# Optimization experiments

Hardware: AMD Instinct MI355X
Metric: run time of the kernel (lower is better)

Reference implementation:

```python
import jax, jax.numpy as jnp
from jax import lax
import numpy as np

B, T, ID, HD = 64, 256, 512, 1024

def setup_inputs() -> dict:
    key = jax.random.key(0)
    ks = jax.random.split(key, 5)
    s_i = 1.0 / np.sqrt(ID)
    s_h = 1.0 / np.sqrt(HD)
    return {
        'x': jax.random.normal(ks[0], (B, T, ID), jnp.float32),
        'Wi': jax.random.uniform(ks[1], (ID, 4 * HD), jnp.float32, -s_i, s_i),
        'bi': jax.random.uniform(ks[2], (4 * HD,), jnp.float32, -s_i, s_i),
        'Wh': jax.random.uniform(ks[3], (HD, 4 * HD), jnp.float32, -s_h, s_h),
        'bh': jax.random.uniform(ks[4], (4 * HD,), jnp.float32, -s_h, s_h),
    }

def reference(x, Wi, bi, Wh, bh):
    # x: [B, T, ID]; Wi: [ID, 4H]; Wh: [HD, 4H]
    b, t, _ = x.shape
    hd = Wh.shape[0]
    # Precompute input-to-hidden contribution for all timesteps: [T, B, 4H]
    gates_x = jnp.swapaxes(jnp.einsum('bti,ih->bth', x, Wi) + bi, 0, 1)

    def step(carry, gx):
        h, c = carry
        g = gx + h @ Wh + bh  # [B, 4H]
        f, i, a, o = jnp.split(g, 4, axis=-1)  # chunk order: F, I, A, O
        f = jax.nn.sigmoid(f)
        i = jax.nn.sigmoid(i)
        a = jnp.tanh(a)
        o = jax.nn.sigmoid(o)
        c = f * c + i * a
        h = o * jnp.tanh(c)
        return (h, c), h

    h0 = jnp.zeros((b, hd), x.dtype)
    c0 = jnp.zeros((b, hd), x.dtype)
    (hT, cT), hs = lax.scan(step, (h0, c0), gates_x)
    Q_all = jnp.swapaxes(hs, 0, 1)  # [B, T, HD]
    return (Q_all, hT, cT)
```

## Files before the change

### kernel.cpp

```cpp
#include <hip/hip_runtime.h>
#include <hip/hip_bf16.h>


#define B_  64
#define T_  256
#define ID_ 512
#define HD_ 1024
#define NG_ 4096
#define M1_ (B_ * T_)
#define NBLK 128
#define UPB  8

typedef __bf16 bf16x8 __attribute__((ext_vector_type(8)));
typedef float  f32x4  __attribute__((ext_vector_type(4)));
typedef int    i32x4  __attribute__((ext_vector_type(4)));
typedef int    i32x2  __attribute__((ext_vector_type(2)));
typedef short  s16x4  __attribute__((ext_vector_type(4)));

using bf16 = __hip_bfloat16;

__device__ __forceinline__ float sigmoid_fast(float x) {
    return 1.0f / (1.0f + __expf(-x));
}
__device__ __forceinline__ float tanh_fast(float x) {
    return 1.0f - 2.0f / (__expf(2.0f * x) + 1.0f);
}
__device__ __forceinline__ unsigned short bf16_bits(float x) {
    union { bf16 h; unsigned short u; } cv;
    cv.h = __float2bfloat16(x);
    return cv.u;
}
__device__ __forceinline__ bf16x8 as_bf16x8(i32x4 v) {
    union { i32x4 i; bf16x8 h; } cv;
    cv.i = v;
    return cv.h;
}

__device__ __forceinline__ void issue8(i32x4* dst, const bf16* gbase) {
    asm volatile(
        "global_load_dwordx4 %0, %8, off sc0 sc1\n\t"
        "global_load_dwordx4 %1, %8, off offset:64 sc0 sc1\n\t"
        "global_load_dwordx4 %2, %8, off offset:128 sc0 sc1\n\t"
        "global_load_dwordx4 %3, %8, off offset:192 sc0 sc1\n\t"
        "global_load_dwordx4 %4, %8, off offset:256 sc0 sc1\n\t"
        "global_load_dwordx4 %5, %8, off offset:320 sc0 sc1\n\t"
        "global_load_dwordx4 %6, %8, off offset:384 sc0 sc1\n\t"
        "global_load_dwordx4 %7, %8, off offset:448 sc0 sc1"
        : "=&v"(dst[0]), "=&v"(dst[1]), "=&v"(dst[2]), "=&v"(dst[3]),
          "=&v"(dst[4]), "=&v"(dst[5]), "=&v"(dst[6]), "=&v"(dst[7])
        : "v"(gbase));
}

__global__ __launch_bounds__(256) void prep_kernel(
    const float* __restrict__ x, const float* __restrict__ Wi,
    const float* __restrict__ Wh, bf16* __restrict__ xb,
    bf16* __restrict__ wiT, bf16* __restrict__ whT,
    bf16* __restrict__ hbuf, int* __restrict__ flags) {
    const int tid = blockIdx.x * 256 + threadIdx.x;

    if (tid < NBLK * 4 * 16) flags[tid] = 0;
    if (tid < (B_ * HD_) / 4)
        *reinterpret_cast<s16x4*>(hbuf + (size_t)tid * 4) = s16x4{0, 0, 0, 0};

    const float4 v = reinterpret_cast<const float4*>(x)[tid];
    bf16 tmp[4] = { __float2bfloat16(v.x), __float2bfloat16(v.y),
                    __float2bfloat16(v.z), __float2bfloat16(v.w) };
    *reinterpret_cast<s16x4*>(xb + 4 * (size_t)tid) =
        *reinterpret_cast<s16x4*>(tmp);

    {
        const int n = tid >> 9, k = tid & 511;
        wiT[tid] = __float2bfloat16(Wi[(size_t)k * NG_ + n]);
    }
    for (int e = 0; e < 2; ++e) {
        const int idx = 2 * tid + e;
        const int n = idx >> 10, k = idx & 1023;
        whT[idx] = __float2bfloat16(Wh[(size_t)k * NG_ + n]);
    }
}

__global__ __launch_bounds__(256) void gates_gemm_kernel(
    const bf16* __restrict__ xb, const bf16* __restrict__ wiT,
    const float* __restrict__ bi, const float* __restrict__ bh,
    bf16* __restrict__ gates3) {
    __shared__ __align__(16) bf16 As[128 * 40];
    __shared__ __align__(16) bf16 Bs[128 * 40];
    const int tid  = threadIdx.x;
    const int lane = tid & 63, wave = tid >> 6;
    const int wm = wave >> 1, wn = wave & 1;
    const int l15 = lane & 15, quad = lane >> 4;
    const int row0 = blockIdx.x * 128, col0 = blockIdx.y * 128;

    f32x4 acc[4][4];
    for (int i = 0; i < 4; ++i)
        for (int j = 0; j < 4; ++j) acc[i][j] = f32x4{0.f, 0.f, 0.f, 0.f};

    for (int kt = 0; kt < ID_ / 32; ++kt) {
        const int k0 = kt * 32;
        for (int L = tid; L < 512; L += 256) {
            const int r = L >> 2, s = L & 3;
            *reinterpret_cast<i32x4*>(&As[r * 40 + s * 8]) =
                *reinterpret_cast<const i32x4*>(xb + (size_t)(row0 + r) * ID_ + k0 + s * 8);
            *reinterpret_cast<i32x4*>(&Bs[r * 40 + s * 8]) =
                *reinterpret_cast<const i32x4*>(wiT + (size_t)(col0 + r) * ID_ + k0 + s * 8);
        }
        __syncthreads();
        bf16x8 af[4], bfv[4];
        for (int mt = 0; mt < 4; ++mt)
            af[mt] = *reinterpret_cast<const bf16x8*>(
                &As[(wm * 64 + mt * 16 + l15) * 40 + quad * 8]);
        for (int nt = 0; nt < 4; ++nt)
            bfv[nt] = *reinterpret_cast<const bf16x8*>(
                &Bs[(wn * 64 + nt * 16 + l15) * 40 + quad * 8]);
        for (int mt = 0; mt < 4; ++mt)
            for (int nt = 0; nt < 4; ++nt)
                acc[mt][nt] = __builtin_amdgcn_mfma_f32_16x16x32_bf16(
                    af[mt], bfv[nt], acc[mt][nt], 0, 0, 0);
        __syncthreads();
    }
    for (int mt = 0; mt < 4; ++mt) {
        for (int nt = 0; nt < 4; ++nt) {
            const int cg = col0 + wn * 64 + nt * 16 + l15;
            const int g = cg >> 10, u = cg & 1023;
            const int blk = u >> 3, jl = u & 7;
            const int lcol = g * 8 + jl;
            const int nt2 = lcol >> 4, q2 = (lcol >> 2) & 3, r2 = lcol & 3;
            const int e = nt2 * 4 + r2;
            const float bias = bi[cg] + bh[cg];
            for (int r = 0; r < 4; ++r) {
                const int rg = row0 + wm * 64 + mt * 16 + quad * 4 + r;
                const int b = rg >> 8, t = rg & 255;
                const int tid2 = (b >> 4) * 64 + q2 * 16 + (b & 15);
                gates3[(((size_t)t * NBLK + blk) * 256 + tid2) * 8 + e] =
                    __float2bfloat16(acc[mt][nt][r] + bias);
            }
        }
    }
}

__global__ __launch_bounds__(256, 1) void lstm_persistent_kernel(
    const bf16* __restrict__ gates3, const bf16* __restrict__ whT,
    bf16* __restrict__ hbuf, float* __restrict__ out, int* __restrict__ flags) {
    __shared__ __align__(16) bf16 whs[32 * 2 * 64 * 8];
    const int tid  = threadIdx.x;
    const int lane = tid & 63, w = tid >> 6;
    const int l15 = lane & 15, quad = lane >> 4;
    const int blk = blockIdx.x;

    for (int c = tid; c < 4096; c += 256) {
        const int kk = c >> 7, sel = (c >> 6) & 1, ln = c & 63;
        const int m = sel * 16 + (ln & 15);
        const size_t wrow = (size_t)((m >> 3) * HD_ + blk * UPB + (m & 7));
        const int col = (ln >> 4) * 8 + kk * 32;
        *reinterpret_cast<i32x4*>(whs + (size_t)c * 8) =
            *reinterpret_cast<const i32x4*>(whT + wrow * HD_ + col);
    }
    __syncthreads();

    const bf16* wb = whs + (size_t)lane * 8;

    const int jl0 = 4 * (quad & 1) + 2 * (quad >> 1);
    const int b = w * 16 + l15;
    float c0 = 0.f, c1 = 0.f;

    const int* pollp = flags + (lane << 1);

    bf16x8 gx_next = *reinterpret_cast<const bf16x8*>(
        gates3 + ((size_t)blk * 256 + tid) * 8);

    for (int t = 0; t < T_; ++t) {
        const bf16* hin  = hbuf + (size_t)(t & 1) * (B_ * HD_);
        bf16*       hout = hbuf + (size_t)((t + 1) & 1) * (B_ * HD_);
        const bf16x8 gx = gx_next;

        if (t > 0) {
            if (w == 0) {
                for (;;) {
                    i32x2 f = *reinterpret_cast<const volatile i32x2*>(pollp);
                    if (f.x >= t && f.y >= t) break;
                    __builtin_amdgcn_s_sleep(2);
                }
            }
            asm volatile("s_barrier" ::: "memory");
        }

        f32x4 a0e = f32x4{0.f, 0.f, 0.f, 0.f};
        f32x4 a0o = f32x4{0.f, 0.f, 0.f, 0.f};
        f32x4 a1e = f32x4{0.f, 0.f, 0.f, 0.f};
        f32x4 a1o = f32x4{0.f, 0.f, 0.f, 0.f};

        const bf16* hb_base = hin + (size_t)b * HD_ + quad * 8;
        i32x4 hbA[8], hbB[8];

        auto consume8 = [&](const i32x4* hbg, const int kkb) {
#pragma unroll
            for (int i = 0; i < 8; i += 2) {
                const int kk = kkb + i;
                const bf16x8 w0e = *reinterpret_cast<const bf16x8*>(wb + (size_t)kk * 1024);
                const bf16x8 w1e = *reinterpret_cast<const bf16x8*>(wb + (size_t)kk * 1024 + 512);
                const bf16x8 w0o = *reinterpret_cast<const bf16x8*>(wb + (size_t)(kk + 1) * 1024);
                const bf16x8 w1o = *reinterpret_cast<const bf16x8*>(wb + (size_t)(kk + 1) * 1024 + 512);
                a0e = __builtin_amdgcn_mfma_f32_16x16x32_bf16(w0e, as_bf16x8(hbg[i]), a0e, 0, 0, 0);
                a1e = __builtin_amdgcn_mfma_f32_16x16x32_bf16(w1e, as_bf16x8(hbg[i]), a1e, 0, 0, 0);
                a0o = __builtin_amdgcn_mfma_f32_16x16x32_bf16(w0o, as_bf16x8(hbg[i + 1]), a0o, 0, 0, 0);
                a1o = __builtin_amdgcn_mfma_f32_16x16x32_bf16(w1o, as_bf16x8(hbg[i + 1]), a1o, 0, 0, 0);
            }
        };

        issue8(hbA, hb_base);
        issue8(hbB, hb_base + 8 * 32);
        asm volatile("s_waitcnt vmcnt(8)" ::: "memory");
        __builtin_amdgcn_sched_barrier(0);
        consume8(hbA, 0);
        issue8(hbA, hb_base + 16 * 32);
        asm volatile("s_waitcnt vmcnt(8)" ::: "memory");
        __builtin_amdgcn_sched_barrier(0);
        consume8(hbB, 8);
        issue8(hbB, hb_base + 24 * 32);
        asm volatile("s_waitcnt vmcnt(8)" ::: "memory");
        __builtin_amdgcn_sched_barrier(0);
        consume8(hbA, 16);
        asm volatile("s_waitcnt vmcnt(0)" ::: "memory");
        __builtin_amdgcn_sched_barrier(0);
        consume8(hbB, 24);

        const f32x4 acc0 = a0e + a0o;
        const f32x4 acc1 = a1e + a1o;

        float v0[4], v1[4];
#pragma unroll
        for (int r = 0; r < 4; ++r) {
            const float p0 = acc0[r] + (float)gx[r];
            const float p1 = acc1[r] + (float)gx[4 + r];
            v0[r] = sigmoid_fast(p0);
            v1[r] = (quad < 2) ? tanh_fast(p1) : sigmoid_fast(p1);
        }
        float u0[4], u1[4];
#pragma unroll
        for (int r = 0; r < 4; ++r) {
            u0[r] = __shfl_xor(v0[r], 32, 64);
            u1[r] = __shfl_xor(v1[r], 32, 64);
        }
        const int rsel = 2 * (quad >> 1);
        const float f0 = (quad < 2) ? v0[rsel]     : u0[rsel];
        const float i0 = (quad < 2) ? u0[rsel]     : v0[rsel];
        const float a0 = (quad < 2) ? v1[rsel]     : u1[rsel];
        const float o0 = (quad < 2) ? u1[rsel]     : v1[rsel];
        const float f1 = (quad < 2) ? v0[rsel + 1] : u0[rsel + 1];
        const float i1 = (quad < 2) ? u0[rsel + 1] : v0[rsel + 1];
        const float a1 = (quad < 2) ? v1[rsel + 1] : u1[rsel + 1];
        const float o1 = (quad < 2) ? u1[rsel + 1] : v1[rsel + 1];

        const float cn0 = f0 * c0 + i0 * a0;  c0 = cn0;
        const float cn1 = f1 * c1 + i1 * a1;  c1 = cn1;
        const float h0 = o0 * tanh_fast(cn0);
        const float h1 = o1 * tanh_fast(cn1);

        const int hidx = b * HD_ + blk * UPB + jl0;
        *reinterpret_cast<float2*>(
            out + ((size_t)b * T_ + t) * HD_ + blk * UPB + jl0) =
            make_float2(h0, h1);
        if (t == T_ - 1) {
            *reinterpret_cast<float2*>(out + (size_t)M1_ * HD_ + hidx) =
                make_float2(h0, h1);
            *reinterpret_cast<float2*>(
                out + (size_t)M1_ * HD_ + B_ * HD_ + hidx) =
                make_float2(cn0, cn1);
        }
        if (t < T_ - 1) {
            const unsigned int packed =
                (unsigned int)bf16_bits(h0) | ((unsigned int)bf16_bits(h1) << 16);
            *reinterpret_cast<volatile unsigned int*>(hout + hidx) = packed;
            __asm__ __volatile__("s_waitcnt vmcnt(0)" ::: "memory");
            asm volatile("s_barrier" ::: "memory");
            if (tid == 0)
                *reinterpret_cast<volatile int*>(flags + blk) = t + 1;
            __asm__ __volatile__("" ::: "memory");
            gx_next = *reinterpret_cast<const bf16x8*>(
                gates3 + (((size_t)(t + 1) * NBLK + blk) * 256 + tid) * 8);
        }
    }
}

extern "C" void kernel_launch(void* const* d_in, const int* in_sizes, int n_in,
                              void* d_out, int out_size, void* d_ws, size_t ws_size,
                              hipStream_t stream) {
    const float* x  = (const float*)d_in[0];
    const float* Wi = (const float*)d_in[1];
    const float* bi = (const float*)d_in[2];
    const float* Wh = (const float*)d_in[3];
    const float* bh = (const float*)d_in[4];
    float* out = (float*)d_out;

    char* ws = (char*)d_ws;
    size_t off = 0;
    bf16* xb     = (bf16*)(ws + off); off += (size_t)M1_ * ID_ * 2;
    bf16* wiT    = (bf16*)(ws + off); off += (size_t)NG_ * ID_ * 2;
    bf16* whT    = (bf16*)(ws + off); off += (size_t)NG_ * HD_ * 2;
    bf16* gates3 = (bf16*)(ws + off); off += (size_t)T_ * B_ * NG_ * 2;
    bf16* hbuf   = (bf16*)(ws + off); off += (size_t)2 * B_ * HD_ * 2;
    int* flags   = (int*)(ws + off);  off += (size_t)NBLK * 4 * 16 * 4;

    prep_kernel<<<8192, 256, 0, stream>>>(x, Wi, Wh, xb, wiT, whT, hbuf, flags);
    gates_gemm_kernel<<<dim3(128, 32), 256, 0, stream>>>(xb, wiT, bi, bh, gates3);

    lstm_persistent_kernel<<<dim3(NBLK), dim3(256), 0, stream>>>(
        gates3, whT, hbuf, out, flags);
}
```

Before: 2.150 ms.

## Use 64 persistent LSTM blocks with 16 hidden units each

Halves the number of persistent blocks in the recurrent kernel and doubles the hidden units each block owns. Each wave now computes all four gates for its units, so the cross-lane shuffle to regroup gates goes away. Flag polling needs one flag per lane instead of two, and the gate precompute layout is changed to match. The trade is twice the MFMA work and twice the LDS weight footprint per block per step, with fewer blocks to synchronise and less contention on h reads.

```diff
diff --git a/kernel.cpp b/kernel.cpp
--- a/kernel.cpp
+++ b/kernel.cpp
@@ -8,13 +8,12 @@
 #define HD_ 1024
 #define NG_ 4096
 #define M1_ (B_ * T_)
-#define NBLK 128
-#define UPB  8
+#define NBLK 64
+#define UPB  16
 
 typedef __bf16 bf16x8 __attribute__((ext_vector_type(8)));
 typedef float  f32x4  __attribute__((ext_vector_type(4)));
 typedef int    i32x4  __attribute__((ext_vector_type(4)));
-typedef int    i32x2  __attribute__((ext_vector_type(2)));
 typedef short  s16x4  __attribute__((ext_vector_type(4)));
 
 using bf16 = __hip_bfloat16;
@@ -122,16 +121,15 @@
         for (int nt = 0; nt < 4; ++nt) {
             const int cg = col0 + wn * 64 + nt * 16 + l15;
             const int g = cg >> 10, u = cg & 1023;
-            const int blk = u >> 3, jl = u & 7;
-            const int lcol = g * 8 + jl;
-            const int nt2 = lcol >> 4, q2 = (lcol >> 2) & 3, r2 = lcol & 3;
-            const int e = nt2 * 4 + r2;
+            const int blk = u >> 4, ul = u & 15;
+            const int q2 = ul >> 2, r2 = ul & 3;
+            const int e = g * 4 + r2;
             const float bias = bi[cg] + bh[cg];
             for (int r = 0; r < 4; ++r) {
                 const int rg = row0 + wm * 64 + mt * 16 + quad * 4 + r;
                 const int b = rg >> 8, t = rg & 255;
                 const int tid2 = (b >> 4) * 64 + q2 * 16 + (b & 15);
-                gates3[(((size_t)t * NBLK + blk) * 256 + tid2) * 8 + e] =
+                gates3[(((size_t)t * NBLK + blk) * 256 + tid2) * 16 + e] =
                     __float2bfloat16(acc[mt][nt][r] + bias);
             }
         }
@@ -141,16 +139,15 @@
 __global__ __launch_bounds__(256, 1) void lstm_persistent_kernel(
     const bf16* __restrict__ gates3, const bf16* __restrict__ whT,
     bf16* __restrict__ hbuf, float* __restrict__ out, int* __restrict__ flags) {
-    __shared__ __align__(16) bf16 whs[32 * 2 * 64 * 8];
+    __shared__ __align__(16) bf16 whs[32 * 4 * 64 * 8];
     const int tid  = threadIdx.x;
     const int lane = tid & 63, w = tid >> 6;
     const int l15 = lane & 15, quad = lane >> 4;
     const int blk = blockIdx.x;
 
-    for (int c = tid; c < 4096; c += 256) {
-        const int kk = c >> 7, sel = (c >> 6) & 1, ln = c & 63;
-        const int m = sel * 16 + (ln & 15);
-        const size_t wrow = (size_t)((m >> 3) * HD_ + blk * UPB + (m & 7));
+    for (int c = tid; c < 8192; c += 256) {
+        const int kk = c >> 8, sel = (c >> 6) & 3, ln = c & 63;
+        const size_t wrow = (size_t)(sel * HD_ + blk * UPB + (ln & 15));
         const int col = (ln >> 4) * 8 + kk * 32;
         *reinterpret_cast<i32x4*>(whs + (size_t)c * 8) =
             *reinterpret_cast<const i32x4*>(whT + wrow * HD_ + col);
@@ -159,35 +156,31 @@
 
     const bf16* wb = whs + (size_t)lane * 8;
 
-    const int jl0 = 4 * (quad & 1) + 2 * (quad >> 1);
     const int b = w * 16 + l15;
-    float c0 = 0.f, c1 = 0.f;
-
-    const int* pollp = flags + (lane << 1);
-
-    bf16x8 gx_next = *reinterpret_cast<const bf16x8*>(
-        gates3 + ((size_t)blk * 256 + tid) * 8);
+    float cs[4] = {0.f, 0.f, 0.f, 0.f};
+
+    const volatile int* pf = (const volatile int*)(flags + lane);
+
+    size_t gb0 = ((size_t)blk * 256 + tid) * 16;
+    bf16x8 gxa_n = *reinterpret_cast<const bf16x8*>(gates3 + gb0);
+    bf16x8 gxb_n = *reinterpret_cast<const bf16x8*>(gates3 + gb0 + 8);
 
     for (int t = 0; t < T_; ++t) {
         const bf16* hin  = hbuf + (size_t)(t & 1) * (B_ * HD_);
         bf16*       hout = hbuf + (size_t)((t + 1) & 1) * (B_ * HD_);
-        const bf16x8 gx = gx_next;
+        const bf16x8 gxa = gxa_n, gxb = gxb_n;
 
         if (t > 0) {
             if (w == 0) {
-                for (;;) {
-                    i32x2 f = *reinterpret_cast<const volatile i32x2*>(pollp);
-                    if (f.x >= t && f.y >= t) break;
-                    __builtin_amdgcn_s_sleep(2);
-                }
+                while (*pf < t) __builtin_amdgcn_s_sleep(2);
             }
             asm volatile("s_barrier" ::: "memory");
         }
 
-        f32x4 a0e = f32x4{0.f, 0.f, 0.f, 0.f};
-        f32x4 a0o = f32x4{0.f, 0.f, 0.f, 0.f};
-        f32x4 a1e = f32x4{0.f, 0.f, 0.f, 0.f};
-        f32x4 a1o = f32x4{0.f, 0.f, 0.f, 0.f};
+        f32x4 aFe{0.f,0.f,0.f,0.f}, aFo{0.f,0.f,0.f,0.f};
+        f32x4 aIe{0.f,0.f,0.f,0.f}, aIo{0.f,0.f,0.f,0.f};
+        f32x4 aAe{0.f,0.f,0.f,0.f}, aAo{0.f,0.f,0.f,0.f};
+        f32x4 aOe{0.f,0.f,0.f,0.f}, aOo{0.f,0.f,0.f,0.f};
 
         const bf16* hb_base = hin + (size_t)b * HD_ + quad * 8;
         i32x4 hbA[8], hbB[8];
@@ -196,14 +189,26 @@
 #pragma unroll
             for (int i = 0; i < 8; i += 2) {
                 const int kk = kkb + i;
-                const bf16x8 w0e = *reinterpret_cast<const bf16x8*>(wb + (size_t)kk * 1024);
-                const bf16x8 w1e = *reinterpret_cast<const bf16x8*>(wb + (size_t)kk * 1024 + 512);
-                const bf16x8 w0o = *reinterpret_cast<const bf16x8*>(wb + (size_t)(kk + 1) * 1024);
-                const bf16x8 w1o = *reinterpret_cast<const bf16x8*>(wb + (size_t)(kk + 1) * 1024 + 512);
-                a0e = __builtin_amdgcn_mfma_f32_16x16x32_bf16(w0e, as_bf16x8(hbg[i]), a0e, 0, 0, 0);
-                a1e = __builtin_amdgcn_mfma_f32_16x16x32_bf16(w1e, as_bf16x8(hbg[i]), a1e, 0, 0, 0);
-                a0o = __builtin_amdgcn_mfma_f32_16x16x32_bf16(w0o, as_bf16x8(hbg[i + 1]), a0o, 0, 0, 0);
-                a1o = __builtin_amdgcn_mfma_f32_16x16x32_bf16(w1o, as_bf16x8(hbg[i + 1]), a1o, 0, 0, 0);
+                const bf16* f0 = wb + (size_t)kk * 2048;
+                const bf16* f1 = f0 + 2048;
+                const bf16x8 he = as_bf16x8(hbg[i]);
+                const bf16x8 ho = as_bf16x8(hbg[i + 1]);
+                aFe = __builtin_amdgcn_mfma_f32_16x16x32_bf16(
+                    *reinterpret_cast<const bf16x8*>(f0),        he, aFe, 0, 0, 0);
+                aIe = __builtin_amdgcn_mfma_f32_16x16x32_bf16(
+                    *reinterpret_cast<const bf16x8*>(f0 + 512),  he, aIe, 0, 0, 0);
+                aAe = __builtin_amdgcn_mfma_f32_16x16x32_bf16(
+                    *reinterpret_cast<const bf16x8*>(f0 + 1024), he, aAe, 0, 0, 0);
+                aOe = __builtin_amdgcn_mfma_f32_16x16x32_bf16(
+                    *reinterpret_cast<const bf16x8*>(f0 + 1536), he, aOe, 0, 0, 0);
+                aFo = __builtin_amdgcn_mfma_f32_16x16x32_bf16(
+                    *reinterpret_cast<const bf16x8*>(f1),        ho, aFo, 0, 0, 0);
+                aIo = __builtin_amdgcn_mfma_f32_16x16x32_bf16(
+                    *reinterpret_cast<const bf16x8*>(f1 + 512),  ho, aIo, 0, 0, 0);
+                aAo = __builtin_amdgcn_mfma_f32_16x16x32_bf16(
+                    *reinterpret_cast<const bf16x8*>(f1 + 1024), ho, aAo, 0, 0, 0);
+                aOo = __builtin_amdgcn_mfma_f32_16x16x32_bf16(
+                    *reinterpret_cast<const bf16x8*>(f1 + 1536), ho, aOo, 0, 0, 0);
             }
         };
 
@@ -224,60 +229,47 @@
         __builtin_amdgcn_sched_barrier(0);
         consume8(hbB, 24);
 
-        const f32x4 acc0 = a0e + a0o;
-        const f32x4 acc1 = a1e + a1o;
-
-        float v0[4], v1[4];
+        const f32x4 accF = aFe + aFo;
+        const f32x4 accI = aIe + aIo;
+        const f32x4 accA = aAe + aAo;
+        const f32x4 accO = aOe + aOo;
+        float hs[4];
 #pragma unroll
         for (int r = 0; r < 4; ++r) {
-            const float p0 = acc0[r] + (float)gx[r];
-            const float p1 = acc1[r] + (float)gx[4 + r];
-            v0[r] = sigmoid_fast(p0);
-            v1[r] = (quad < 2) ? tanh_fast(p1) : sigmoid_fast(p1);
-        }
-        float u0[4], u1[4];
-#pragma unroll
-        for (int r = 0; r < 4; ++r) {
-            u0[r] = __shfl_xor(v0[r], 32, 64);
-            u1[r] = __shfl_xor(v1[r], 32, 64);
-        }
-        const int rsel = 2 * (quad >> 1);
-        const float f0 = (quad < 2) ? v0[rsel]     : u0[rsel];
-        const float i0 = (quad < 2) ? u0[rsel]     : v0[rsel];
-        const float a0 = (quad < 2) ? v1[rsel]     : u1[rsel];
-        const float o0 = (quad < 2) ? u1[rsel]     : v1[rsel];
-        const float f1 = (quad < 2) ? v0[rsel + 1] : u0[rsel + 1];
-        const float i1 = (quad < 2) ? u0[rsel + 1] : v0[rsel + 1];
-        const float a1 = (quad < 2) ? v1[rsel + 1] : u1[rsel + 1];
-        const float o1 = (quad < 2) ? u1[rsel + 1] : v1[rsel + 1];
-
-        const float cn0 = f0 * c0 + i0 * a0;  c0 = cn0;
-        const float cn1 = f1 * c1 + i1 * a1;  c1 = cn1;
-        const float h0 = o0 * tanh_fast(cn0);
-        const float h1 = o1 * tanh_fast(cn1);
-
-        const int hidx = b * HD_ + blk * UPB + jl0;
-        *reinterpret_cast<float2*>(
-            out + ((size_t)b * T_ + t) * HD_ + blk * UPB + jl0) =
-            make_float2(h0, h1);
+            const float fv = sigmoid_fast(accF[r] + (float)gxa[r]);
+            const float iv = sigmoid_fast(accI[r] + (float)gxa[4 + r]);
+            const float av = tanh_fast   (accA[r] + (float)gxb[r]);
+            const float ov = sigmoid_fast(accO[r] + (float)gxb[4 + r]);
+            cs[r] = fv * cs[r] + iv * av;
+            hs[r] = ov * tanh_fast(cs[r]);
+        }
+
+        const int hidx = b * HD_ + blk * UPB + quad * 4;
+        *reinterpret_cast<float4*>(
+            out + ((size_t)b * T_ + t) * HD_ + blk * UPB + quad * 4) =
+            make_float4(hs[0], hs[1], hs[2], hs[3]);
         if (t == T_ - 1) {
-            *reinterpret_cast<float2*>(out + (size_t)M1_ * HD_ + hidx) =
-                make_float2(h0, h1);
-            *reinterpret_cast<float2*>(
+            *reinterpret_cast<float4*>(out + (size_t)M1_ * HD_ + hidx) =
+                make_float4(hs[0], hs[1], hs[2], hs[3]);
+            *reinterpret_cast<float4*>(
                 out + (size_t)M1_ * HD_ + B_ * HD_ + hidx) =
-                make_float2(cn0, cn1);
+                make_float4(cs[0], cs[1], cs[2], cs[3]);
         }
         if (t < T_ - 1) {
-            const unsigned int packed =
-                (unsigned int)bf16_bits(h0) | ((unsigned int)bf16_bits(h1) << 16);
-            *reinterpret_cast<volatile unsigned int*>(hout + hidx) = packed;
+            const unsigned long long hp =
+                (unsigned long long)bf16_bits(hs[0]) |
+                ((unsigned long long)bf16_bits(hs[1]) << 16) |
+                ((unsigned long long)bf16_bits(hs[2]) << 32) |
+                ((unsigned long long)bf16_bits(hs[3]) << 48);
+            *reinterpret_cast<volatile unsigned long long*>(hout + hidx) = hp;
             __asm__ __volatile__("s_waitcnt vmcnt(0)" ::: "memory");
             asm volatile("s_barrier" ::: "memory");
             if (tid == 0)
                 *reinterpret_cast<volatile int*>(flags + blk) = t + 1;
             __asm__ __volatile__("" ::: "memory");
-            gx_next = *reinterpret_cast<const bf16x8*>(
-                gates3 + (((size_t)(t + 1) * NBLK + blk) * 256 + tid) * 8);
+            const size_t gb = (((size_t)(t + 1) * NBLK + blk) * 256 + tid) * 16;
+            gxa_n = *reinterpret_cast<const bf16x8*>(gates3 + gb);
+            gxb_n = *reinterpret_cast<const bf16x8*>(gates3 + gb + 8);
         }
     }
 }
```

Result: faster. 2.050 ms (-4.6%).
